# Kernel tuning notes

Hardware: AMD Instinct MI355X
Metric: run time of the kernel (lower is better)

Reference implementation:

```python
import jax, jax.numpy as jnp
import numpy as np

EPS = 1e-5

def _layer_norm(y, w, b):
    mu = y.mean(-1, keepdims=True)
    var = jnp.mean((y - mu) ** 2, axis=-1, keepdims=True)
    return (y - mu) * jax.lax.rsqrt(var + EPS) * w + b


def setup_inputs() -> dict:
    key = jax.random.key(0)
    ks = jax.random.split(key, 8)
    B, D, H, W = 1, 96, 96, 96
    N, R, K = 16, 6, 4
    x = jax.random.normal(ks[0], (B, D, H, W), jnp.float32)
    x_proj_weight = jax.random.normal(ks[1], (K, R + 2 * N, D), jnp.float32) * 0.05
    dt_projs_weight = jax.random.normal(ks[2], (K, D, R), jnp.float32) * 0.1
    dt_projs_bias = jax.random.normal(ks[3], (K, D), jnp.float32) * 0.1
    A_logs = jax.random.normal(ks[4], (K * D, N), jnp.float32)
    Ds = jax.random.normal(ks[5], (K * D,), jnp.float32) * 0.1
    ln_w = jnp.ones((D,), jnp.float32)
    ln_b = jnp.zeros((D,), jnp.float32)
    return {"x": x, "x_proj_weight": x_proj_weight, "dt_projs_weight": dt_projs_weight,
            "dt_projs_bias": dt_projs_bias, "A_logs": A_logs, "Ds": Ds,
            "ln_w": ln_w, "ln_b": ln_b}


def reference(x, x_proj_weight, dt_projs_weight, dt_projs_bias, A_logs, Ds, ln_w, ln_b):
    B, D, H, W = x.shape
    L = H * W
    K = x_proj_weight.shape[0]            # 4 scan directions
    N = A_logs.shape[1]                   # d_state
    R = dt_projs_weight.shape[2]          # dt_rank

    # ---- CrossScan: 4 directional flattenings -> xs [B, K, D, L]
    xs0 = x.reshape(B, D, L)
    xs1 = jnp.swapaxes(x, 2, 3).reshape(B, D, L)
    xs = jnp.stack([xs0, xs1, xs0[:, :, ::-1], xs1[:, :, ::-1]], axis=1)

    # ---- input-dependent projections
    x_dbl = jnp.einsum('bkdl,kcd->bkcl', xs, x_proj_weight)    # [B,K,R+2N,L]
    dts = x_dbl[:, :, :R]
    Bs = x_dbl[:, :, R:R + N]                                  # [B,K,N,L]
    Cs = x_dbl[:, :, R + N:]                                   # [B,K,N,L]
    dts = jnp.einsum('bkrl,kdr->bkdl', dts, dt_projs_weight)   # [B,K,D,L]

    # ---- selective scan (S6), delta_softplus=True, fp32
    delta = jax.nn.softplus(dts + dt_projs_bias[None, :, :, None])   # [B,K,D,L]
    A = -jnp.exp(A_logs).reshape(K, D, N)                             # [K,D,N]
    dA = jnp.exp(jnp.einsum('bkdl,kdn->bkdln', delta, A))             # [B,K,D,L,N]
    dBu = jnp.einsum('bkdl,bknl,bkdl->bkdln', delta, Bs, xs)          # delta*B*u

    def combine(c1, c2):
        a1, b1 = c1
        a2, b2 = c2
        return a1 * a2, a2 * b1 + b2

    _, h = jax.lax.associative_scan(combine, (dA, dBu), axis=3)       # h_t over L

    y = jnp.einsum('bkdln,bknl->bkdl', h, Cs)
    y = y + xs * Ds.reshape(K, D)[None, :, :, None]                   # [B,K,D,L]

    # ---- CrossMerge: undo the 4 directional scans and sum
    ys = y[:, 0:2] + y[:, 2:4, :, ::-1]                               # [B,2,D,L]
    ym = ys[:, 0] + jnp.swapaxes(ys[:, 1].reshape(B, D, W, H), 2, 3).reshape(B, D, L)

    # ---- out_norm (LayerNorm over D) and reshape to [B,H,W,D]
    yout = jnp.swapaxes(ym, 1, 2)                                     # [B,L,D]
    yout = _layer_norm(yout, ln_w, ln_b).reshape(B, H, W, D)
    return yout.astype(x.dtype)
```

## Files before the change

kernel.cpp:

```cpp
#include <hip/hip_runtime.h>
#include <math.h>

constexpr int cD = 96, cL = 9216, cK = 4;
constexpr int CL = 36, NCH = 256;
constexpr long cDL = (long)cD * cL;
constexpr float LOG2E = 1.44269504088896f;

constexpr long OFF_XT    = 0;
constexpr long OFF_DELTA = OFF_XT    + cDL;
constexpr long OFF_BC    = OFF_DELTA + 4L*cDL;
constexpr long OFF_Y     = OFF_BC    + 4L*cL*32;
constexpr long OFF_YT    = OFF_Y     + 4L*cDL;
constexpr long OFF_PG    = OFF_YT    + 2L*cDL;
constexpr long OFF_SG    = OFF_PG    + 384L*256*16;

__device__ __forceinline__ float4 a2prep(float4 v) {
    return make_float4(-LOG2E * exp2f(LOG2E * v.x), -LOG2E * exp2f(LOG2E * v.y),
                       -LOG2E * exp2f(LOG2E * v.z), -LOG2E * exp2f(LOG2E * v.w));
}
template<int C>
__device__ __forceinline__ float qperm(float v) {
    return __int_as_float(__builtin_amdgcn_mov_dpp(__float_as_int(v), C, 0xf, 0xf, true));
}

__global__ __launch_bounds__(256) void kT(const float* __restrict__ x,
                                          float* __restrict__ xT) {
    __shared__ float t[32][33];
    const int h0 = blockIdx.x * 32, w0 = blockIdx.y * 32, d = blockIdx.z;
    const float* xd = x + (long)d * cL;
    float* xtd = xT + (long)d * cL;
    for (int o = threadIdx.x; o < 1024; o += 256) {
        int i = o >> 5, j = o & 31;
        t[i][j] = xd[(h0 + i) * 96 + w0 + j];
    }
    __syncthreads();
    for (int o = threadIdx.x; o < 1024; o += 256) {
        int i = o >> 5, j = o & 31;
        xtd[(w0 + i) * 96 + h0 + j] = t[j][i];
    }
}

__global__ __launch_bounds__(256) void kA(const float* __restrict__ x,
                                          const float* __restrict__ xT,
                                          const float* __restrict__ xpw,
                                          const float* __restrict__ dtw,
                                          const float* __restrict__ dtb,
                                          float* __restrict__ delta,
                                          float* __restrict__ BC) {
    __shared__ float xs[96][64];
    __shared__ float xdbl[38][65];
    __shared__ float dtw_l[96 * 6];
    __shared__ float dtb_l[96];
    const int p0 = blockIdx.x * 64;
    const int k  = blockIdx.y;
    const int tid = threadIdx.x;
    const float* src = (k & 1) ? xT : x;

    for (int o = tid; o < 96 * 64; o += 256) {
        int dd = o >> 6, pp = o & 63;
        xs[dd][pp] = src[(long)dd * cL + p0 + pp];
    }
    for (int o = tid; o < 96 * 6; o += 256) dtw_l[o] = dtw[k * 96 * 6 + o];
    if (tid < 96) dtb_l[tid] = dtb[k * 96 + tid];
    __syncthreads();

    const int lane = tid & 63;
    const int c0 = __builtin_amdgcn_readfirstlane((tid >> 6) * 10);
    const float* wk = xpw + (long)k * 38 * 96;
    float acc[10];
    #pragma unroll
    for (int i = 0; i < 10; ++i) acc[i] = 0.f;
    #pragma unroll 4
    for (int dd = 0; dd < 96; ++dd) {
        float xv = xs[dd][lane];
        #pragma unroll
        for (int i = 0; i < 10; ++i) {
            int c = c0 + i; c = c > 37 ? 37 : c;
            acc[i] = fmaf(xv, wk[c * 96 + dd], acc[i]);
        }
    }
    #pragma unroll
    for (int i = 0; i < 10; ++i) {
        int c = c0 + i; c = c > 37 ? 37 : c;
        xdbl[c][lane] = acc[i];
    }
    __syncthreads();

    for (int o = tid; o < 64 * 16; o += 256) {
        int n = o & 15, pp = o >> 4;
        int P = p0 + pp;
        int q = (k < 2) ? P : (9215 - P);
        int ch = q / 36, j = q - ch * 36;
        int g = j >> 2, r = j & 3;
        long idx = ((((long)k * 9 + g) * 256 + ch) * 4 + r) * 32 + n;
        BC[idx]      = xdbl[6 + n][pp];
        BC[idx + 16] = xdbl[22 + n][pp];
    }
    for (int o = tid; o < 96 * 64; o += 256) {
        int dd = o >> 6, pp = o & 63;
        float s = dtb_l[dd];
        #pragma unroll
        for (int r = 0; r < 6; ++r) s = fmaf(xdbl[r][pp], dtw_l[dd * 6 + r], s);
        float sp = fmaxf(s, 0.f) + __logf(1.f + __expf(-fabsf(s)));
        delta[((long)(k * 96 + dd)) * cL + p0 + pp] = sp;
    }
}

__global__ __launch_bounds__(512, 6) void kS1(const float* __restrict__ x,
                                              const float* __restrict__ xT,
                                              const float* __restrict__ delta,
                                              const float* __restrict__ BC,
                                              const float* __restrict__ Alog,
                                              float* __restrict__ Pg,
                                              float* __restrict__ Sg) {
    const int tid = threadIdx.x;
    const int n0 = (tid & 3) * 4, chl = tid >> 2;
    const int hb = blockIdx.x & 1, seq = blockIdx.x >> 1;
    const int k = seq / 96, d = seq % 96, rev = k >> 1;
    const int ch = hb * 128 + chl;
    const int q0 = ch * CL;

    const float4 a2 = a2prep(*(const float4*)(Alog + (long)seq * 16 + n0));
    const float* dRow = delta + (long)seq * cL;
    const float* xRow = ((k & 1) ? xT : x) + (long)d * cL;
    const float* bc0 = BC + ((long)k * 9 * 256 * 4 + (long)ch * 4) * 32 + n0;

    float4 h = make_float4(0.f, 0.f, 0.f, 0.f);
    float sdl = 0.f;
#define ST(DL, XV, BPTR, ROFF) { \
        float4 B = *(const float4*)((BPTR) + (ROFF) * 32); \
        float t = (DL) * (XV); sdl += (DL); \
        h.x = fmaf(exp2f((DL)*a2.x), h.x, t*B.x); \
        h.y = fmaf(exp2f((DL)*a2.y), h.y, t*B.y); \
        h.z = fmaf(exp2f((DL)*a2.z), h.z, t*B.z); \
        h.w = fmaf(exp2f((DL)*a2.w), h.w, t*B.w); }
    #pragma unroll
    for (int g = 0; g < 9; ++g) {
        const float* bg = bc0 + (long)g * 32768;
        if (!rev) {
            float4 d4 = *(const float4*)(dRow + q0 + 4 * g);
            float4 x4 = *(const float4*)(xRow + q0 + 4 * g);
            ST(d4.x, x4.x, bg, 0) ST(d4.y, x4.y, bg, 1)
            ST(d4.z, x4.z, bg, 2) ST(d4.w, x4.w, bg, 3)
        } else {
            float4 d4 = *(const float4*)(dRow + 9212 - q0 - 4 * g);
            float4 x4 = *(const float4*)(xRow + 9212 - q0 - 4 * g);
            ST(d4.w, x4.w, bg, 0) ST(d4.z, x4.z, bg, 1)
            ST(d4.y, x4.y, bg, 2) ST(d4.x, x4.x, bg, 3)
        }
    }
#undef ST
    long o = ((long)seq * NCH + ch) * 16 + n0;
    *(float4*)(Pg + o) = make_float4(exp2f(a2.x*sdl), exp2f(a2.y*sdl),
                                     exp2f(a2.z*sdl), exp2f(a2.w*sdl));
    *(float4*)(Sg + o) = h;
}

__global__ __launch_bounds__(512, 6) void kS2(const float* __restrict__ x,
                                              const float* __restrict__ xT,
                                              const float* __restrict__ delta,
                                              const float* __restrict__ BC,
                                              const float* __restrict__ Alog,
                                              const float* __restrict__ Dsv,
                                              const float* __restrict__ Pg,
                                              const float* __restrict__ Sg,
                                              float* __restrict__ y) {
    __shared__ float lp[NCH][16];
    __shared__ float ls[NCH][16];
    float* gpf = &lp[0][0];
    const int tid = threadIdx.x;
    const int hb = blockIdx.x & 1, seq = blockIdx.x >> 1;
    const int k = seq / 96, d = seq % 96, rev = k >> 1;

    #pragma unroll
    for (int i = 0; i < 8; ++i) {
        ((float*)lp)[tid + i * 512] = Pg[(long)seq * 4096 + tid + i * 512];
        ((float*)ls)[tid + i * 512] = Sg[(long)seq * 4096 + tid + i * 512];
    }
    __syncthreads();

    const int sn = tid & 15, sg = tid >> 4;
    float LPe[8], LSe[8];
    {
        float P = 1.f, S = 0.f;
        #pragma unroll
        for (int i = 0; i < 8; ++i) {
            LPe[i] = P; LSe[i] = S;
            float p = lp[sg * 8 + i][sn], s = ls[sg * 8 + i][sn];
            S = fmaf(p, S, s); P = p * P;
        }
        __syncthreads();
        gpf[tid] = P; gpf[512 + tid] = S;
    }
    __syncthreads();
    #pragma unroll
    for (int off = 1; off < 32; off <<= 1) {
        float pc = gpf[tid], sc = gpf[512 + tid];
        float pn = pc, snn = sc;
        if (sg >= off) {
            pn  = pc * gpf[tid - off * 16];
            snn = fmaf(pc, gpf[512 + tid - off * 16], sc);
        }
        __syncthreads();
        gpf[tid] = pn; gpf[512 + tid] = snn;
        __syncthreads();
    }
    const float GS = (sg == 0) ? 0.f : gpf[512 + tid - 16];
    #pragma unroll
    for (int i = 0; i < 8; ++i) ls[sg * 8 + i][sn] = fmaf(LPe[i], GS, LSe[i]);
    __syncthreads();

    const int n0 = (tid & 3) * 4, chl = tid >> 2;
    const int r = tid & 3;
    const int ch = hb * 128 + chl;
    const int q0 = ch * CL;
    const float4 a2 = a2prep(*(const float4*)(Alog + (long)seq * 16 + n0));
    const float Dv = Dsv[seq];
    const float* dRow = delta + (long)seq * cL;
    const float* xRow = ((k & 1) ? xT : x) + (long)d * cL;
    const float* bc0 = BC + ((long)k * 9 * 256 * 4 + (long)ch * 4) * 32 + n0;
    float4 h = *(float4*)&ls[ch][n0];
    float* yq = y + (long)seq * cL + q0;
    float yhold = 0.f;

#define ST(DL, XV, BPTR, ROFF, SI) { \
        float4 B = *(const float4*)((BPTR) + (ROFF) * 32); \
        float4 C = *(const float4*)((BPTR) + (ROFF) * 32 + 16); \
        float t = (DL) * (XV); \
        h.x = fmaf(exp2f((DL)*a2.x), h.x, t*B.x); \
        h.y = fmaf(exp2f((DL)*a2.y), h.y, t*B.y); \
        h.z = fmaf(exp2f((DL)*a2.z), h.z, t*B.z); \
        h.w = fmaf(exp2f((DL)*a2.w), h.w, t*B.w); \
        float pv = fmaf(h.x, C.x, fmaf(h.y, C.y, fmaf(h.z, C.z, h.w * C.w))); \
        pv += qperm<0xB1>(pv); \
        pv += qperm<0x4E>(pv); \
        if ((SI) == r) yhold = fmaf(Dv, (XV), pv); }
    #pragma unroll
    for (int g = 0; g < 9; ++g) {
        const float* bg = bc0 + (long)g * 32768;
        if (!rev) {
            float4 d4 = *(const float4*)(dRow + q0 + 4 * g);
            float4 x4 = *(const float4*)(xRow + q0 + 4 * g);
            ST(d4.x, x4.x, bg, 0, 0) ST(d4.y, x4.y, bg, 1, 1)
            ST(d4.z, x4.z, bg, 2, 2) ST(d4.w, x4.w, bg, 3, 3)
        } else {
            float4 d4 = *(const float4*)(dRow + 9212 - q0 - 4 * g);
            float4 x4 = *(const float4*)(xRow + 9212 - q0 - 4 * g);
            ST(d4.w, x4.w, bg, 0, 0) ST(d4.z, x4.z, bg, 1, 1)
            ST(d4.y, x4.y, bg, 2, 2) ST(d4.x, x4.x, bg, 3, 3)
        }
        yq[4 * g + r] = yhold;
    }
#undef ST
}

__global__ __launch_bounds__(256) void kU(const float* __restrict__ Y,
                                          float* __restrict__ YT) {
    __shared__ float t[32][33];
    const int i0 = blockIdx.x * 32, j0 = blockIdx.y * 32;
    const int z = blockIdx.z;
    const int arr = z / 96, d = z % 96;
    const float* src = Y + (1 + 2 * arr) * cDL + (long)d * cL;
    float* dst = YT + (long)arr * cDL + (long)d * cL;
    for (int o = threadIdx.x; o < 1024; o += 256) {
        int i = o >> 5, j = o & 31;
        t[i][j] = src[(i0 + i) * 96 + j0 + j];
    }
    __syncthreads();
    for (int o = threadIdx.x; o < 1024; o += 256) {
        int i = o >> 5, j = o & 31;
        dst[(j0 + i) * 96 + i0 + j] = t[j][i];
    }
}

__global__ __launch_bounds__(256) void kE(const float* __restrict__ Y,
                                          const float* __restrict__ YT,
                                          const float* __restrict__ lnw,
                                          const float* __restrict__ lnb,
                                          float* __restrict__ out) {
    __shared__ float vs[96][36];
    __shared__ float red[8][32], red2[8][32];
    __shared__ float MU[32], RS[32];
    const int tid = threadIdx.x;
    const int p0 = blockIdx.x * 32;

    for (int o = tid; o < 96 * 8; o += 256) {
        int dd = o >> 3, j = o & 7;
        const float* r0 = Y + (long)dd * cL + p0;
        const float* r1 = YT + (long)dd * cL + p0;
        const float* r2 = Y + 2 * cDL + (long)dd * cL;
        const float* r3 = YT + cDL + (long)dd * cL;
        float4 a = ((const float4*)r0)[j];
        float4 b = ((const float4*)r1)[j];
        float4 c = *(const float4*)(r2 + 9212 - p0 - 4 * j);
        float4 e = *(const float4*)(r3 + 9212 - p0 - 4 * j);
        *(float4*)&vs[dd][4 * j] = make_float4(a.x + b.x + c.w + e.w,
                                               a.y + b.y + c.z + e.z,
                                               a.z + b.z + c.y + e.y,
                                               a.w + b.w + c.x + e.x);
    }
    __syncthreads();

    const int p = tid & 31, part = tid >> 5;
    float s = 0.f, s2 = 0.f;
    for (int dd = part * 12; dd < part * 12 + 12; ++dd) {
        float v = vs[dd][p];
        s += v; s2 = fmaf(v, v, s2);
    }
    red[part][p] = s; red2[part][p] = s2;
    __syncthreads();
    if (tid < 32) {
        float S = 0.f, S2 = 0.f;
        #pragma unroll
        for (int q = 0; q < 8; ++q) { S += red[q][tid]; S2 += red2[q][tid]; }
        float m = S * (1.f / 96.f);
        MU[tid] = m;
        RS[tid] = rsqrtf(S2 * (1.f / 96.f) - m * m + 1e-5f);
    }
    __syncthreads();
    for (int o = tid; o < 32 * 96; o += 256) {
        int pl = o / 96, dd = o - pl * 96;
        out[(long)(p0 + pl) * 96 + dd] = (vs[dd][pl] - MU[pl]) * RS[pl] * lnw[dd] + lnb[dd];
    }
}

extern "C" void kernel_launch(void* const* d_in, const int* in_sizes, int n_in,
                              void* d_out, int out_size, void* d_ws, size_t ws_size,
                              hipStream_t stream) {
    const float* x    = (const float*)d_in[0];
    const float* xpw  = (const float*)d_in[1];
    const float* dtw  = (const float*)d_in[2];
    const float* dtb  = (const float*)d_in[3];
    const float* Alog = (const float*)d_in[4];
    const float* Dsv  = (const float*)d_in[5];
    const float* lnw  = (const float*)d_in[6];
    const float* lnb  = (const float*)d_in[7];
    float* ws = (float*)d_ws;

    float* xT    = ws + OFF_XT;
    float* delta = ws + OFF_DELTA;
    float* BC    = ws + OFF_BC;
    float* y     = ws + OFF_Y;
    float* yT    = ws + OFF_YT;
    float* Pg    = ws + OFF_PG;
    float* Sg    = ws + OFF_SG;
    float* out   = (float*)d_out;

    kT<<<dim3(3, 3, 96), 256, 0, stream>>>(x, xT);
    kA<<<dim3(144, 4), 256, 0, stream>>>(x, xT, xpw, dtw, dtb, delta, BC);
    kS1<<<768, 512, 0, stream>>>(x, xT, delta, BC, Alog, Pg, Sg);
    kS2<<<768, 512, 0, stream>>>(x, xT, delta, BC, Alog, Dsv, Pg, Sg, y);
    kU<<<dim3(3, 3, 192), 256, 0, stream>>>(y, yT);
    kE<<<288, 256, 0, stream>>>(y, yT, lnw, lnb, out);
}
```

Measured before the change: 111.4 us.

## Fuse cross-merge un-transpose and reversal into scan epilogue via LDS staging

The second scan kernel now stages its outputs in shared memory and writes them back already reversed and transposed into the canonical spatial layout. This removes the separate transpose kernel kU and its yT buffer, and lets the LayerNorm kernel read all four directions contiguously. The BC layout is also reorganized to [k][j][ch] so that adjacent chunks read contiguous B/C vectors, with all four step loads hoisted per group. Launch-bound occupancy hints are lowered, which trades fewer waves for more registers, and the added LDS buffer may further limit occupancy.

```diff
diff --git a/kernel.cpp b/kernel.cpp
--- a/kernel.cpp
+++ b/kernel.cpp
@@ -10,8 +10,7 @@
 constexpr long OFF_DELTA = OFF_XT    + cDL;
 constexpr long OFF_BC    = OFF_DELTA + 4L*cDL;
 constexpr long OFF_Y     = OFF_BC    + 4L*cL*32;
-constexpr long OFF_YT    = OFF_Y     + 4L*cDL;
-constexpr long OFF_PG    = OFF_YT    + 2L*cDL;
+constexpr long OFF_PG    = OFF_Y     + 4L*cDL;
 constexpr long OFF_SG    = OFF_PG    + 384L*256*16;
 
 __device__ __forceinline__ float4 a2prep(float4 v) {
@@ -91,8 +90,7 @@
         int P = p0 + pp;
         int q = (k < 2) ? P : (9215 - P);
         int ch = q / 36, j = q - ch * 36;
-        int g = j >> 2, r = j & 3;
-        long idx = ((((long)k * 9 + g) * 256 + ch) * 4 + r) * 32 + n;
+        long idx = (((long)k * 36 + j) * 256 + ch) * 32 + n;
         BC[idx]      = xdbl[6 + n][pp];
         BC[idx + 16] = xdbl[22 + n][pp];
     }
@@ -106,7 +104,7 @@
     }
 }
 
-__global__ __launch_bounds__(512, 6) void kS1(const float* __restrict__ x,
+__global__ __launch_bounds__(512, 5) void kS1(const float* __restrict__ x,
                                               const float* __restrict__ xT,
                                               const float* __restrict__ delta,
                                               const float* __restrict__ BC,
@@ -123,40 +121,44 @@
     const float4 a2 = a2prep(*(const float4*)(Alog + (long)seq * 16 + n0));
     const float* dRow = delta + (long)seq * cL;
     const float* xRow = ((k & 1) ? xT : x) + (long)d * cL;
-    const float* bc0 = BC + ((long)k * 9 * 256 * 4 + (long)ch * 4) * 32 + n0;
+    const float* bc = BC + ((long)k * 36 * 256 + ch) * 32 + n0;
 
     float4 h = make_float4(0.f, 0.f, 0.f, 0.f);
     float sdl = 0.f;
-#define ST(DL, XV, BPTR, ROFF) { \
-        float4 B = *(const float4*)((BPTR) + (ROFF) * 32); \
+#define STEP1(DL, XV, B) { \
         float t = (DL) * (XV); sdl += (DL); \
-        h.x = fmaf(exp2f((DL)*a2.x), h.x, t*B.x); \
-        h.y = fmaf(exp2f((DL)*a2.y), h.y, t*B.y); \
-        h.z = fmaf(exp2f((DL)*a2.z), h.z, t*B.z); \
-        h.w = fmaf(exp2f((DL)*a2.w), h.w, t*B.w); }
+        h.x = fmaf(exp2f((DL)*a2.x), h.x, t*(B).x); \
+        h.y = fmaf(exp2f((DL)*a2.y), h.y, t*(B).y); \
+        h.z = fmaf(exp2f((DL)*a2.z), h.z, t*(B).z); \
+        h.w = fmaf(exp2f((DL)*a2.w), h.w, t*(B).w); }
     #pragma unroll
     for (int g = 0; g < 9; ++g) {
-        const float* bg = bc0 + (long)g * 32768;
+        const float* bj = bc + (long)(4 * g) * 8192;
+        float4 B0 = *(const float4*)(bj);
+        float4 B1 = *(const float4*)(bj + 8192);
+        float4 B2 = *(const float4*)(bj + 16384);
+        float4 B3 = *(const float4*)(bj + 24576);
+        float4 d4, x4;
         if (!rev) {
-            float4 d4 = *(const float4*)(dRow + q0 + 4 * g);
-            float4 x4 = *(const float4*)(xRow + q0 + 4 * g);
-            ST(d4.x, x4.x, bg, 0) ST(d4.y, x4.y, bg, 1)
-            ST(d4.z, x4.z, bg, 2) ST(d4.w, x4.w, bg, 3)
+            d4 = *(const float4*)(dRow + q0 + 4 * g);
+            x4 = *(const float4*)(xRow + q0 + 4 * g);
+            STEP1(d4.x, x4.x, B0) STEP1(d4.y, x4.y, B1)
+            STEP1(d4.z, x4.z, B2) STEP1(d4.w, x4.w, B3)
         } else {
-            float4 d4 = *(const float4*)(dRow + 9212 - q0 - 4 * g);
-            float4 x4 = *(const float4*)(xRow + 9212 - q0 - 4 * g);
-            ST(d4.w, x4.w, bg, 0) ST(d4.z, x4.z, bg, 1)
-            ST(d4.y, x4.y, bg, 2) ST(d4.x, x4.x, bg, 3)
-        }
-    }
-#undef ST
+            d4 = *(const float4*)(dRow + 9212 - q0 - 4 * g);
+            x4 = *(const float4*)(xRow + 9212 - q0 - 4 * g);
+            STEP1(d4.w, x4.w, B0) STEP1(d4.z, x4.z, B1)
+            STEP1(d4.y, x4.y, B2) STEP1(d4.x, x4.x, B3)
+        }
+    }
+#undef STEP1
     long o = ((long)seq * NCH + ch) * 16 + n0;
     *(float4*)(Pg + o) = make_float4(exp2f(a2.x*sdl), exp2f(a2.y*sdl),
                                      exp2f(a2.z*sdl), exp2f(a2.w*sdl));
     *(float4*)(Sg + o) = h;
 }
 
-__global__ __launch_bounds__(512, 6) void kS2(const float* __restrict__ x,
+__global__ __launch_bounds__(512, 3) void kS2(const float* __restrict__ x,
                                               const float* __restrict__ xT,
                                               const float* __restrict__ delta,
                                               const float* __restrict__ BC,
@@ -167,6 +169,7 @@
                                               float* __restrict__ y) {
     __shared__ float lp[NCH][16];
     __shared__ float ls[NCH][16];
+    __shared__ float ybuf[4608 + 48];
     float* gpf = &lp[0][0];
     const int tid = threadIdx.x;
     const int hb = blockIdx.x & 1, seq = blockIdx.x >> 1;
@@ -214,67 +217,71 @@
     const int r = tid & 3;
     const int ch = hb * 128 + chl;
     const int q0 = ch * CL;
+    const int slB = chl * CL;
     const float4 a2 = a2prep(*(const float4*)(Alog + (long)seq * 16 + n0));
     const float Dv = Dsv[seq];
     const float* dRow = delta + (long)seq * cL;
     const float* xRow = ((k & 1) ? xT : x) + (long)d * cL;
-    const float* bc0 = BC + ((long)k * 9 * 256 * 4 + (long)ch * 4) * 32 + n0;
+    const float* bc = BC + ((long)k * 36 * 256 + ch) * 32 + n0;
     float4 h = *(float4*)&ls[ch][n0];
-    float* yq = y + (long)seq * cL + q0;
     float yhold = 0.f;
 
-#define ST(DL, XV, BPTR, ROFF, SI) { \
-        float4 B = *(const float4*)((BPTR) + (ROFF) * 32); \
-        float4 C = *(const float4*)((BPTR) + (ROFF) * 32 + 16); \
+#define STEP2(DL, XV, B, C, SI) { \
         float t = (DL) * (XV); \
-        h.x = fmaf(exp2f((DL)*a2.x), h.x, t*B.x); \
-        h.y = fmaf(exp2f((DL)*a2.y), h.y, t*B.y); \
-        h.z = fmaf(exp2f((DL)*a2.z), h.z, t*B.z); \
-        h.w = fmaf(exp2f((DL)*a2.w), h.w, t*B.w); \
-        float pv = fmaf(h.x, C.x, fmaf(h.y, C.y, fmaf(h.z, C.z, h.w * C.w))); \
+        h.x = fmaf(exp2f((DL)*a2.x), h.x, t*(B).x); \
+        h.y = fmaf(exp2f((DL)*a2.y), h.y, t*(B).y); \
+        h.z = fmaf(exp2f((DL)*a2.z), h.z, t*(B).z); \
+        h.w = fmaf(exp2f((DL)*a2.w), h.w, t*(B).w); \
+        float pv = fmaf(h.x, (C).x, fmaf(h.y, (C).y, fmaf(h.z, (C).z, h.w * (C).w))); \
         pv += qperm<0xB1>(pv); \
         pv += qperm<0x4E>(pv); \
         if ((SI) == r) yhold = fmaf(Dv, (XV), pv); }
     #pragma unroll
     for (int g = 0; g < 9; ++g) {
-        const float* bg = bc0 + (long)g * 32768;
+        const float* bj = bc + (long)(4 * g) * 8192;
+        float4 B0 = *(const float4*)(bj);
+        float4 C0 = *(const float4*)(bj + 16);
+        float4 B1 = *(const float4*)(bj + 8192);
+        float4 C1 = *(const float4*)(bj + 8192 + 16);
+        float4 B2 = *(const float4*)(bj + 16384);
+        float4 C2 = *(const float4*)(bj + 16384 + 16);
+        float4 B3 = *(const float4*)(bj + 24576);
+        float4 C3 = *(const float4*)(bj + 24576 + 16);
+        float4 d4, x4;
         if (!rev) {
-            float4 d4 = *(const float4*)(dRow + q0 + 4 * g);
-            float4 x4 = *(const float4*)(xRow + q0 + 4 * g);
-            ST(d4.x, x4.x, bg, 0, 0) ST(d4.y, x4.y, bg, 1, 1)
-            ST(d4.z, x4.z, bg, 2, 2) ST(d4.w, x4.w, bg, 3, 3)
+            d4 = *(const float4*)(dRow + q0 + 4 * g);
+            x4 = *(const float4*)(xRow + q0 + 4 * g);
+            STEP2(d4.x, x4.x, B0, C0, 0) STEP2(d4.y, x4.y, B1, C1, 1)
+            STEP2(d4.z, x4.z, B2, C2, 2) STEP2(d4.w, x4.w, B3, C3, 3)
         } else {
-            float4 d4 = *(const float4*)(dRow + 9212 - q0 - 4 * g);
-            float4 x4 = *(const float4*)(xRow + 9212 - q0 - 4 * g);
-            ST(d4.w, x4.w, bg, 0, 0) ST(d4.z, x4.z, bg, 1, 1)
-            ST(d4.y, x4.y, bg, 2, 2) ST(d4.x, x4.x, bg, 3, 3)
-        }
-        yq[4 * g + r] = yhold;
-    }
-#undef ST
-}
-
-__global__ __launch_bounds__(256) void kU(const float* __restrict__ Y,
-                                          float* __restrict__ YT) {
-    __shared__ float t[32][33];
-    const int i0 = blockIdx.x * 32, j0 = blockIdx.y * 32;
-    const int z = blockIdx.z;
-    const int arr = z / 96, d = z % 96;
-    const float* src = Y + (1 + 2 * arr) * cDL + (long)d * cL;
-    float* dst = YT + (long)arr * cDL + (long)d * cL;
-    for (int o = threadIdx.x; o < 1024; o += 256) {
-        int i = o >> 5, j = o & 31;
-        t[i][j] = src[(i0 + i) * 96 + j0 + j];
-    }
-    __syncthreads();
-    for (int o = threadIdx.x; o < 1024; o += 256) {
-        int i = o >> 5, j = o & 31;
-        dst[(j0 + i) * 96 + i0 + j] = t[j][i];
-    }
-}
-
-__global__ __launch_bounds__(256) void kE(const float* __restrict__ Y,
-                                          const float* __restrict__ YT,
+            d4 = *(const float4*)(dRow + 9212 - q0 - 4 * g);
+            x4 = *(const float4*)(xRow + 9212 - q0 - 4 * g);
+            STEP2(d4.w, x4.w, B0, C0, 0) STEP2(d4.z, x4.z, B1, C1, 1)
+            STEP2(d4.y, x4.y, B2, C2, 2) STEP2(d4.x, x4.x, B3, C3, 3)
+        }
+        int sl = slB + 4 * g + r;
+        int yloc = rev ? 4607 - sl : sl;
+        ybuf[yloc + yloc / 96] = yhold;
+    }
+#undef STEP2
+    __syncthreads();
+
+    const int sb = rev ? (1 - hb) * 4608 : hb * 4608;
+    float* yrow = y + (long)seq * cL;
+    if (k & 1) {
+        const int w0 = sb / 96;
+        for (int o = tid; o < 4608; o += 512) {
+            int hh = o / 48, wl = o - hh * 48;
+            yrow[hh * 96 + w0 + wl] = ybuf[wl * 97 + hh];
+        }
+    } else {
+        for (int o = tid; o < 4608; o += 512) {
+            yrow[sb + o] = ybuf[o + o / 96];
+        }
+    }
+}
+
+__global__ __launch_bounds__(256) void kE(const float* __restrict__ y,
                                           const float* __restrict__ lnw,
                                           const float* __restrict__ lnb,
                                           float* __restrict__ out) {
@@ -286,18 +293,18 @@
 
     for (int o = tid; o < 96 * 8; o += 256) {
         int dd = o >> 3, j = o & 7;
-        const float* r0 = Y + (long)dd * cL + p0;
-        const float* r1 = YT + (long)dd * cL + p0;
-        const float* r2 = Y + 2 * cDL + (long)dd * cL;
-        const float* r3 = YT + cDL + (long)dd * cL;
+        const float* r0 = y + (long)dd * cL + p0;
+        const float* r1 = y + cDL + (long)dd * cL + p0;
+        const float* r2 = y + 2 * cDL + (long)dd * cL + p0;
+        const float* r3 = y + 3 * cDL + (long)dd * cL + p0;
         float4 a = ((const float4*)r0)[j];
         float4 b = ((const float4*)r1)[j];
-        float4 c = *(const float4*)(r2 + 9212 - p0 - 4 * j);
-        float4 e = *(const float4*)(r3 + 9212 - p0 - 4 * j);
-        *(float4*)&vs[dd][4 * j] = make_float4(a.x + b.x + c.w + e.w,
-                                               a.y + b.y + c.z + e.z,
-                                               a.z + b.z + c.y + e.y,
-                                               a.w + b.w + c.x + e.x);
+        float4 c = ((const float4*)r2)[j];
+        float4 e = ((const float4*)r3)[j];
+        *(float4*)&vs[dd][4 * j] = make_float4(a.x + b.x + c.x + e.x,
+                                               a.y + b.y + c.y + e.y,
+                                               a.z + b.z + c.z + e.z,
+                                               a.w + b.w + c.w + e.w);
     }
     __syncthreads();
 
@@ -341,7 +348,6 @@
     float* delta = ws + OFF_DELTA;
     float* BC    = ws + OFF_BC;
     float* y     = ws + OFF_Y;
-    float* yT    = ws + OFF_YT;
     float* Pg    = ws + OFF_PG;
     float* Sg    = ws + OFF_SG;
     float* out   = (float*)d_out;
@@ -350,6 +356,5 @@
     kA<<<dim3(144, 4), 256, 0, stream>>>(x, xT, xpw, dtw, dtb, delta, BC);
     kS1<<<768, 512, 0, stream>>>(x, xT, delta, BC, Alog, Pg, Sg);
     kS2<<<768, 512, 0, stream>>>(x, xT, delta, BC, Alog, Dsv, Pg, Sg, y);
-    kU<<<dim3(3, 3, 192), 256, 0, stream>>>(y, yT);
-    kE<<<288, 256, 0, stream>>>(y, yT, lnw, lnb, out);
-}
+    kE<<<288, 256, 0, stream>>>(y, lnw, lnb, out);
+}
```

After: 97.43 us. 12.5% less time.
